# Optimization experiments

Hardware: AMD Instinct MI355X
Metric: run time of the kernel (lower is better)

Reference implementation:

```python
import jax, jax.numpy as jnp
import numpy as np

N_NODES = 100000


def _mean_agg(feat, src, dst, n):
    # segment mean of neighbor messages: h_N[v] = mean_{(u->v) in E} feat[u]
    s = jax.ops.segment_sum(feat[src], dst, num_segments=n)  # [n, d]
    cnt = jax.ops.segment_sum(jnp.ones_like(src, dtype=feat.dtype), dst, num_segments=n)
    return s / jnp.maximum(cnt, 1.0)[:, None]  # isolated nodes -> 0 (DGL mean gives 0)


def setup_inputs() -> dict:
    key = jax.random.key(0)
    k1, k2, k3, k4, k5 = jax.random.split(key, 5)
    n, d_in, d_hid, d_out, n_edges = N_NODES, 128, 128, 64, 1600000
    feat = jax.random.normal(k1, (n, d_in), dtype=jnp.float32)
    edge_src = jax.random.randint(k2, (n_edges,), 0, n, dtype=jnp.int32)
    edge_dst = jax.random.randint(k3, (n_edges,), 0, n, dtype=jnp.int32)
    # xavier_uniform with relu gain, torch Linear weight layout [out, in]
    gain = float(np.sqrt(2.0))
    def xavier(k, out_f, in_f):
        bound = gain * np.sqrt(6.0 / (in_f + out_f))
        return jax.random.uniform(k, (out_f, in_f), minval=-bound, maxval=bound, dtype=jnp.float32)
    W0 = xavier(k4, d_hid, 2 * d_in)
    W1 = xavier(k5, d_out, 2 * d_hid)
    return {"feat": feat, "edge_src": edge_src, "edge_dst": edge_dst, "W0": W0, "W1": W1}


def reference(feat, edge_src, edge_dst, W0, W1):
    n = feat.shape[0]
    # layer 0: mean-aggregate, concat, linear, relu (dropout p=0 -> identity)
    h_N = _mean_agg(feat, edge_src, edge_dst, n)
    h = jax.nn.relu(jnp.concatenate([feat, h_N], axis=1) @ W0.T)
    # final layer: mean-aggregate, concat, linear (no relu)
    h_N2 = _mean_agg(h, edge_src, edge_dst, n)
    out = jnp.concatenate([h, h_N2], axis=1) @ W1.T
    return out
```

## Files before the change

kernel.cpp:

```cpp
#include <hip/hip_runtime.h>
#include <hip/hip_bf16.h>

typedef __attribute__((ext_vector_type(8))) short bf16x8;
typedef __attribute__((ext_vector_type(4))) float f32x4;
typedef __attribute__((ext_vector_type(2))) float f32x2;

#define BSH 9
#define BCAP 12288

#if __has_builtin(__builtin_amdgcn_cvt_pk_f32_fp8) && __has_builtin(__builtin_amdgcn_cvt_pk_fp8_f32)
#define FP8_HW 1
#else
#define FP8_HW 0
#endif

__device__ __forceinline__ float bf2f(unsigned short u) {
    return __uint_as_float(((unsigned int)u) << 16);
}
__device__ __forceinline__ unsigned short f2bf(float f) {
    unsigned int u = __float_as_uint(f);
    unsigned int r = u + 0x7FFFu + ((u >> 16) & 1u);
    return (unsigned short)(r >> 16);
}
__device__ __forceinline__ unsigned int pack2bf(float a, float b) {
    return (unsigned int)f2bf(a) | ((unsigned int)f2bf(b) << 16);
}

#if !FP8_HW
__device__ __forceinline__ unsigned int f2fp8_sw(float v) {
    unsigned int u = __float_as_uint(v);
    unsigned int s = (u >> 24) & 0x80u;
    unsigned int a = u & 0x7FFFFFFFu;
    float av = __uint_as_float(a);
    unsigned int q;
    if (av >= 0.015625f) {
        unsigned int r = a + 0x7FFFFu + ((a >> 20) & 1u);
        q = (r - (120u << 23)) >> 20;
        if (q > 0x7Eu) q = 0x7Eu;
    } else {
        q = (unsigned int)(av * 512.0f + 0.5f);
    }
    return s | q;
}
__device__ __forceinline__ float fp8_dec_sw(unsigned int u8) {
    unsigned int s = (u8 & 0x80u) << 24;
    unsigned int em = u8 & 0x7Fu;
    float vn = __uint_as_float(s | ((em << 20) + (120u << 23)));
    float vs = __uint_as_float(s | 0x3B000000u) * (float)(int)em;
    return em >= 8 ? vn : vs;
}
#endif

__device__ __forceinline__ void fp8x4_dec(unsigned int d, float& x, float& y, float& z, float& w) {
#if FP8_HW
    f32x2 lo = __builtin_amdgcn_cvt_pk_f32_fp8((int)d, false);
    f32x2 hi = __builtin_amdgcn_cvt_pk_f32_fp8((int)d, true);
    x = lo.x; y = lo.y; z = hi.x; w = hi.y;
#else
    x = fp8_dec_sw(d & 0xFFu);
    y = fp8_dec_sw((d >> 8) & 0xFFu);
    z = fp8_dec_sw((d >> 16) & 0xFFu);
    w = fp8_dec_sw((d >> 24) & 0xFFu);
#endif
}
__device__ __forceinline__ unsigned int fp8x4_enc(float a, float b, float c, float d) {
#if FP8_HW
    int u = __builtin_amdgcn_cvt_pk_fp8_f32(a, b, 0, false);
    u = __builtin_amdgcn_cvt_pk_fp8_f32(c, d, u, true);
    return (unsigned int)u;
#else
    return f2fp8_sw(a) | (f2fp8_sw(b) << 8) | (f2fp8_sw(c) << 16) | (f2fp8_sw(d) << 24);
#endif
}
__device__ __forceinline__ unsigned char fp8_enc1(float a) {
#if FP8_HW
    return (unsigned char)(__builtin_amdgcn_cvt_pk_fp8_f32(a, a, 0, false) & 0xFF);
#else
    return (unsigned char)f2fp8_sw(a);
#endif
}

__global__ __launch_bounds__(256) void megaA(const int* __restrict__ esrc, const int* __restrict__ edst,
                                             int* __restrict__ gcur, unsigned int* __restrict__ pairs,
                                             int E, int NB,
                                             const float* __restrict__ feat,
                                             unsigned char* __restrict__ Ff8, int nquad,
                                             const float* __restrict__ W0, unsigned short* __restrict__ Wb1,
                                             const float* __restrict__ W1, unsigned short* __restrict__ Wb2,
                                             int pblocks, int cblocks) {
    __shared__ int bcnt[256];
    __shared__ int bbas[256];
    int b = blockIdx.x, t = threadIdx.x;
    if (b < pblocks) {
        int e0 = b * 4096;
        int eend = min(e0 + 4096, E);
        if (t < NB) bcnt[t] = 0;
        __syncthreads();
        for (int e = e0 + t; e < eend; e += 256) atomicAdd(&bcnt[edst[e] >> BSH], 1);
        __syncthreads();
        if (t < NB) {
            bbas[t] = t * BCAP + atomicAdd(&gcur[t], bcnt[t]);
            bcnt[t] = 0;
        }
        __syncthreads();
        for (int e = e0 + t; e < eend; e += 256) {
            int d = edst[e];
            int s = esrc[e];
            int bk = d >> BSH;
            int off = atomicAdd(&bcnt[bk], 1);
            pairs[bbas[bk] + off] = (unsigned int)s | ((unsigned int)(d & ((1 << BSH) - 1)) << 17);
        }
    } else if (b < pblocks + cblocks) {
        int cb = b - pblocks;
        for (int q = cb * 256 + t; q < nquad; q += cblocks * 256) {
            float4 f = *(const float4*)(feat + (size_t)q * 4);
            *(unsigned int*)(Ff8 + (size_t)q * 4) = fp8x4_enc(f.x, f.y, f.z, f.w);
        }
    } else {
        int wb = b - pblocks - cblocks;
        for (int i = wb * 256 + t; i < 49152; i += 24 * 256) {
            if (i < 32768) {
                Wb1[i] = f2bf(W0[i]);
            } else {
                int i2 = i - 32768;
                int j = i2 >> 7, k = i2 & 127;
                float vv = (j < 64) ? W1[j * 256 + k] : W1[(j - 64) * 256 + 128 + k];
                Wb2[i2] = f2bf(vv);
            }
        }
    }
}

__global__ __launch_bounds__(256) void build(const unsigned int* __restrict__ pairs,
                                             const int* __restrict__ gcur,
                                             int* __restrict__ offs, int* __restrict__ csr,
                                             int n, int NB, int E) {
    __shared__ int cnt[512];
    __shared__ int excl[512];
    __shared__ int wsum[4];
    __shared__ int woff[4];
    __shared__ int sbase;
    int b = blockIdx.x, t = threadIdx.x, lane = t & 63, wv = t >> 6;

    {
        int vv = (t < NB) ? gcur[t] : 0;
        int x = vv;
#pragma unroll
        for (int o = 1; o < 64; o <<= 1) {
            int y = __shfl_up(x, o, 64);
            if (lane >= o) x += y;
        }
        if (lane == 63) wsum[wv] = x;
        __syncthreads();
        if (t == 0) {
            int r = 0;
            for (int w = 0; w < 4; ++w) { woff[w] = r; r += wsum[w]; }
        }
        __syncthreads();
        if (t == b) sbase = woff[wv] + x - vv;
        if (b == 0 && t == 0) offs[n] = E;
    }
    __syncthreads();
    int base = sbase;
    int p0 = b * BCAP;
    int m = gcur[b];
    int v0 = b << BSH;

    cnt[t] = 0;
    cnt[t + 256] = 0;
    __syncthreads();
    for (int i = t; i < m; i += 256) atomicAdd(&cnt[pairs[p0 + i] >> 17], 1);
    __syncthreads();
    int c0 = cnt[2 * t], c1 = cnt[2 * t + 1];
    int s = c0 + c1;
    int x = s;
#pragma unroll
    for (int o = 1; o < 64; o <<= 1) {
        int y = __shfl_up(x, o, 64);
        if (lane >= o) x += y;
    }
    if (lane == 63) wsum[wv] = x;
    __syncthreads();
    if (t == 0) {
        int r = 0;
        for (int w = 0; w < 4; ++w) { woff[w] = r; r += wsum[w]; }
    }
    __syncthreads();
    int ex = woff[wv] + x - s;
    excl[2 * t] = ex;
    excl[2 * t + 1] = ex + c0;
    int v = v0 + 2 * t;
    if (v + 1 < n) {
        int2 o2;
        o2.x = base + ex;
        o2.y = base + ex + c0;
        *(int2*)(offs + v) = o2;
    } else if (v < n) {
        offs[v] = base + ex;
    }
    cnt[t] = 0;
    cnt[t + 256] = 0;
    __syncthreads();
    for (int i = t; i < m; i += 256) {
        unsigned int u = pairs[p0 + i];
        int dl = u >> 17;
        int off = atomicAdd(&cnt[dl], 1);
        csr[base + excl[dl] + off] = (int)(u & 0x1FFFFu);
    }
}

__global__ __launch_bounds__(256) void agg1(const unsigned char* __restrict__ Ff8,
                                            const int* __restrict__ offs,
                                            const int* __restrict__ csr,
                                            unsigned short* __restrict__ Mb, int n) {
    int t = threadIdx.x;
    int hw = t >> 5, cl = t & 31;
    int v = blockIdx.x * 8 + hw;
    if (v >= n) return;
    int beg = offs[v], end = offs[v + 1];
    float a0 = 0.f, a1 = 0.f, a2 = 0.f, a3 = 0.f;
    int e = beg;
    for (; e + 7 < end; e += 8) {
        int s[8];
#pragma unroll
        for (int k = 0; k < 8; ++k) s[k] = csr[e + k];
        unsigned int d[8];
#pragma unroll
        for (int k = 0; k < 8; ++k)
            d[k] = *(const unsigned int*)(Ff8 + (size_t)s[k] * 128 + cl * 4);
#pragma unroll
        for (int k = 0; k < 8; ++k) {
            float x, y, z, w2;
            fp8x4_dec(d[k], x, y, z, w2);
            a0 += x; a1 += y; a2 += z; a3 += w2;
        }
    }
    for (; e < end; ++e) {
        unsigned int d0 = *(const unsigned int*)(Ff8 + (size_t)csr[e] * 128 + cl * 4);
        float x, y, z, w2;
        fp8x4_dec(d0, x, y, z, w2);
        a0 += x; a1 += y; a2 += z; a3 += w2;
    }
    int deg = end - beg;
    float inv = 1.0f / (float)(deg > 0 ? deg : 1);
    uint2 pk;
    pk.x = pack2bf(a0 * inv, a1 * inv);
    pk.y = pack2bf(a2 * inv, a3 * inv);
    *(uint2*)(Mb + (size_t)v * 128 + cl * 4) = pk;
}

__global__ __launch_bounds__(256) void fused_gemm(const float* __restrict__ feat,
                                                  const unsigned short* __restrict__ Mb,
                                                  const unsigned short* __restrict__ Wb1,
                                                  const unsigned short* __restrict__ Wc,
                                                  unsigned short* __restrict__ Za,
                                                  unsigned char* __restrict__ Zb8,
                                                  int n) {
    __shared__ __align__(16) unsigned char smem[32768];
    int t = threadIdx.x, l = t & 63, w = t >> 6;
    int m0 = blockIdx.x * 128;
    int lr = l & 15;
    int lk = (l >> 4) * 8;
    int rbase = (l >> 4) * 4;

    f32x4 acc2[2][8];
    {
        f32x4 acc[2][8];
#pragma unroll
        for (int m = 0; m < 2; ++m)
#pragma unroll
            for (int nf = 0; nf < 8; ++nf) acc[m][nf] = (f32x4){0.f, 0.f, 0.f, 0.f};
#pragma unroll
        for (int kc = 0; kc < 8; ++kc) {
            int kb = kc * 32 + lk;
            bf16x8 a[2];
#pragma unroll
            for (int m = 0; m < 2; ++m) {
                int grow = m0 + w * 32 + m * 16 + lr;
                grow = (grow < n) ? grow : (n - 1);
                if (kb < 128) {
                    float4 f0 = *(const float4*)(feat + (size_t)grow * 128 + kb);
                    float4 f1 = *(const float4*)(feat + (size_t)grow * 128 + kb + 4);
                    uint4 pk;
                    pk.x = pack2bf(f0.x, f0.y);
                    pk.y = pack2bf(f0.z, f0.w);
                    pk.z = pack2bf(f1.x, f1.y);
                    pk.w = pack2bf(f1.z, f1.w);
                    a[m] = *(const bf16x8*)&pk;
                } else {
                    a[m] = *(const bf16x8*)(Mb + (size_t)grow * 128 + (kb - 128));
                }
            }
            bf16x8 bfr[8];
#pragma unroll
            for (int nf = 0; nf < 8; ++nf)
                bfr[nf] = *(const bf16x8*)(Wb1 + (size_t)(nf * 16 + lr) * 256 + kb);
#pragma unroll
            for (int m = 0; m < 2; ++m)
#pragma unroll
                for (int nf = 0; nf < 8; ++nf)
                    acc[m][nf] = __builtin_amdgcn_mfma_f32_16x16x32_bf16(a[m], bfr[nf], acc[m][nf], 0, 0, 0);
        }
#pragma unroll
        for (int m = 0; m < 2; ++m)
#pragma unroll
            for (int nf = 0; nf < 8; ++nf)
#pragma unroll
                for (int r = 0; r < 4; ++r) {
                    int row = w * 32 + m * 16 + rbase + r;
                    int cb = (nf * 16 + lr) * 2;
                    *(unsigned short*)(smem + row * 256 + (cb ^ ((row & 7) << 4))) =
                        f2bf(fmaxf(acc[m][nf][r], 0.f));
                }

#pragma unroll
        for (int m = 0; m < 2; ++m)
#pragma unroll
            for (int nf = 0; nf < 8; ++nf) acc2[m][nf] = (f32x4){0.f, 0.f, 0.f, 0.f};
#pragma unroll
        for (int kc = 0; kc < 4; ++kc) {
            int kb = kc * 32 + lk;
            int cb = kb * 2;
            bf16x8 a[2];
#pragma unroll
            for (int m = 0; m < 2; ++m) {
                int row = w * 32 + m * 16 + lr;
                a[m] = *(const bf16x8*)(smem + row * 256 + (cb ^ ((row & 7) << 4)));
            }
            bf16x8 bfr[8];
#pragma unroll
            for (int nf = 0; nf < 8; ++nf)
                bfr[nf] = *(const bf16x8*)(Wc + (size_t)(nf * 16 + lr) * 128 + kb);
#pragma unroll
            for (int m = 0; m < 2; ++m)
#pragma unroll
                for (int nf = 0; nf < 8; ++nf)
                    acc2[m][nf] = __builtin_amdgcn_mfma_f32_16x16x32_bf16(a[m], bfr[nf], acc2[m][nf], 0, 0, 0);
        }
    }
    __syncthreads();

    {
        unsigned char* zaT = smem;
        unsigned char* zbT = smem + 16384;
#pragma unroll
        for (int m = 0; m < 2; ++m)
#pragma unroll
            for (int nf = 0; nf < 8; ++nf)
#pragma unroll
                for (int r = 0; r < 4; ++r) {
                    float vv = acc2[m][nf][r];
                    int row = w * 32 + m * 16 + rbase + r;
                    if (nf < 4)
                        *(unsigned short*)(zaT + row * 128 + (nf * 16 + lr) * 2) = f2bf(vv);
                    else
                        zbT[row * 64 + (nf - 4) * 16 + lr] = fp8_enc1(vv);
                }
    }
    __syncthreads();

#pragma unroll
    for (int c = 0; c < 4; ++c) {
        int chunk = c * 256 + t;
        int row = chunk >> 3, cb = (chunk & 7) * 16;
        int grow = m0 + row;
        if (grow < n)
            *(uint4*)((unsigned char*)Za + (size_t)grow * 128 + cb) = *(const uint4*)(smem + row * 128 + cb);
    }
#pragma unroll
    for (int c = 0; c < 2; ++c) {
        int chunk = c * 256 + t;
        int row = chunk >> 2, cb = (chunk & 3) * 16;
        int grow = m0 + row;
        if (grow < n)
            *(uint4*)(Zb8 + (size_t)grow * 64 + cb) = *(const uint4*)(smem + 16384 + row * 64 + cb);
    }
}

__global__ __launch_bounds__(256) void agg2(const unsigned short* __restrict__ Za,
                                            const unsigned char* __restrict__ Zb8,
                                            const int* __restrict__ offs,
                                            const int* __restrict__ csr,
                                            float* __restrict__ out, int n) {
    int t = threadIdx.x;
    int q = t >> 4, cl = t & 15;
    int v = blockIdx.x * 16 + q;
    if (v >= n) return;
    int beg = offs[v], end = offs[v + 1];
    float a0 = 0.f, a1 = 0.f, a2 = 0.f, a3 = 0.f;
    int e = beg;
    for (; e + 7 < end; e += 8) {
        int s[8];
#pragma unroll
        for (int k = 0; k < 8; ++k) s[k] = csr[e + k];
        unsigned int d[8];
#pragma unroll
        for (int k = 0; k < 8; ++k)
            d[k] = *(const unsigned int*)(Zb8 + (size_t)s[k] * 64 + cl * 4);
#pragma unroll
        for (int k = 0; k < 8; ++k) {
            float x, y, z, u2;
            fp8x4_dec(d[k], x, y, z, u2);
            a0 += x; a1 += y; a2 += z; a3 += u2;
        }
    }
    for (; e < end; ++e) {
        unsigned int d0 = *(const unsigned int*)(Zb8 + (size_t)csr[e] * 64 + cl * 4);
        float x, y, z, u2;
        fp8x4_dec(d0, x, y, z, u2);
        a0 += x; a1 += y; a2 += z; a3 += u2;
    }
    int deg = end - beg;
    float inv = 1.0f / (float)(deg > 0 ? deg : 1);
    uint2 uz = *(const uint2*)((const unsigned char*)Za + (size_t)v * 128 + cl * 8);
    float4 o;
    o.x = bf2f((unsigned short)uz.x) + a0 * inv;
    o.y = bf2f((unsigned short)(uz.x >> 16)) + a1 * inv;
    o.z = bf2f((unsigned short)uz.y) + a2 * inv;
    o.w = bf2f((unsigned short)(uz.y >> 16)) + a3 * inv;
    *(float4*)(out + (size_t)v * 64 + cl * 4) = o;
}

extern "C" void kernel_launch(void* const* d_in, const int* in_sizes, int n_in,
                              void* d_out, int out_size, void* d_ws, size_t ws_size,
                              hipStream_t stream) {
    const float* feat = (const float*)d_in[0];
    const int* esrc = (const int*)d_in[1];
    const int* edst = (const int*)d_in[2];
    const float* W0 = (const float*)d_in[3];
    const float* W1 = (const float*)d_in[4];
    float* out = (float*)d_out;

    int n = in_sizes[0] / 128;
    int E = in_sizes[1];
    int NB = (n + 511) >> 9;

    char* ws = (char*)d_ws;
    size_t off = 0;
    auto alloc = [&](size_t bytes) -> void* {
        void* p = ws + off;
        off += (bytes + 255) & ~(size_t)255;
        return p;
    };
    int* offs = (int*)alloc((size_t)(n + 1) * 4);
    int* csr = (int*)alloc((size_t)E * 4);
    int* gcur = (int*)alloc((size_t)NB * 4);
    unsigned int* pairs = (unsigned int*)alloc((size_t)NB * BCAP * 4);
    unsigned short* Wb1 = (unsigned short*)alloc((size_t)128 * 256 * 2);
    unsigned short* Wb2 = (unsigned short*)alloc((size_t)128 * 128 * 2);
    unsigned char* Ff8 = (unsigned char*)alloc((size_t)n * 128);
    unsigned short* Mb = (unsigned short*)alloc((size_t)n * 128 * 2);
    unsigned short* Za = (unsigned short*)alloc((size_t)n * 64 * 2);
    unsigned char* Zb8 = (unsigned char*)alloc((size_t)n * 64);

    int pblocks = (E + 4095) / 4096;
    int cblocks = 640;
    int nquad = n * 32;

    hipMemsetAsync(gcur, 0, (size_t)NB * 4, stream);
    megaA<<<pblocks + cblocks + 24, 256, 0, stream>>>(esrc, edst, gcur, pairs, E, NB,
                                                      feat, Ff8, nquad,
                                                      W0, Wb1, W1, Wb2, pblocks, cblocks);
    build<<<NB, 256, 0, stream>>>(pairs, gcur, offs, csr, n, NB, E);

    agg1<<<(n + 7) / 8, 256, 0, stream>>>(Ff8, offs, csr, Mb, n);
    fused_gemm<<<(n + 127) / 128, 256, 0, stream>>>(feat, Mb, Wb1, Wb2, Za, Zb8, n);
    agg2<<<(n + 15) / 16, 256, 0, stream>>>(Za, Zb8, offs, csr, out, n);
}
```

Baseline: 190.9 us.

## Precompute bf16 features and restructure fused GEMM with transposed MFMA and 64-row tiles

The feature-conversion pass now also writes a bf16 copy of the input features, so the fused GEMM reads bf16 directly instead of converting fp32 per tile. The GEMM is restructured to use 64-node tiles with one 16-row fragment per wave, swapping MFMA operands so weights are the A operand. This lets results be packed as contiguous vectors into swizzled shared memory, and the output staging now uses packed fp8 encoding. It adds an extra bf16 feature buffer, which costs one more write and read of the features, while halving shared memory and doubling the block count.

```diff
diff --git a/kernel.cpp b/kernel.cpp
--- a/kernel.cpp
+++ b/kernel.cpp
@@ -72,18 +72,11 @@
     return f2fp8_sw(a) | (f2fp8_sw(b) << 8) | (f2fp8_sw(c) << 16) | (f2fp8_sw(d) << 24);
 #endif
 }
-__device__ __forceinline__ unsigned char fp8_enc1(float a) {
-#if FP8_HW
-    return (unsigned char)(__builtin_amdgcn_cvt_pk_fp8_f32(a, a, 0, false) & 0xFF);
-#else
-    return (unsigned char)f2fp8_sw(a);
-#endif
-}
 
 __global__ __launch_bounds__(256) void megaA(const int* __restrict__ esrc, const int* __restrict__ edst,
                                              int* __restrict__ gcur, unsigned int* __restrict__ pairs,
                                              int E, int NB,
-                                             const float* __restrict__ feat,
+                                             const float* __restrict__ feat, unsigned short* __restrict__ Fb,
                                              unsigned char* __restrict__ Ff8, int nquad,
                                              const float* __restrict__ W0, unsigned short* __restrict__ Wb1,
                                              const float* __restrict__ W1, unsigned short* __restrict__ Wb2,
@@ -114,6 +107,9 @@
         int cb = b - pblocks;
         for (int q = cb * 256 + t; q < nquad; q += cblocks * 256) {
             float4 f = *(const float4*)(feat + (size_t)q * 4);
+            ushort4 ub;
+            ub.x = f2bf(f.x); ub.y = f2bf(f.y); ub.z = f2bf(f.z); ub.w = f2bf(f.w);
+            *(ushort4*)(Fb + (size_t)q * 4) = ub;
             *(unsigned int*)(Ff8 + (size_t)q * 4) = fp8x4_enc(f.x, f.y, f.z, f.w);
         }
     } else {
@@ -249,131 +245,109 @@
     *(uint2*)(Mb + (size_t)v * 128 + cl * 4) = pk;
 }
 
-__global__ __launch_bounds__(256) void fused_gemm(const float* __restrict__ feat,
+__global__ __launch_bounds__(256) void fused_gemm(const unsigned short* __restrict__ Fb,
                                                   const unsigned short* __restrict__ Mb,
                                                   const unsigned short* __restrict__ Wb1,
                                                   const unsigned short* __restrict__ Wc,
                                                   unsigned short* __restrict__ Za,
                                                   unsigned char* __restrict__ Zb8,
                                                   int n) {
-    __shared__ __align__(16) unsigned char smem[32768];
+    __shared__ __align__(16) unsigned char smem[16384];
     int t = threadIdx.x, l = t & 63, w = t >> 6;
-    int m0 = blockIdx.x * 128;
+    int m0 = blockIdx.x * 64;
     int lr = l & 15;
-    int lk = (l >> 4) * 8;
+    int lk8 = (l >> 4) * 8;
     int rbase = (l >> 4) * 4;
 
-    f32x4 acc2[2][8];
-    {
-        f32x4 acc[2][8];
-#pragma unroll
-        for (int m = 0; m < 2; ++m)
-#pragma unroll
-            for (int nf = 0; nf < 8; ++nf) acc[m][nf] = (f32x4){0.f, 0.f, 0.f, 0.f};
-#pragma unroll
-        for (int kc = 0; kc < 8; ++kc) {
-            int kb = kc * 32 + lk;
-            bf16x8 a[2];
-#pragma unroll
-            for (int m = 0; m < 2; ++m) {
-                int grow = m0 + w * 32 + m * 16 + lr;
-                grow = (grow < n) ? grow : (n - 1);
-                if (kb < 128) {
-                    float4 f0 = *(const float4*)(feat + (size_t)grow * 128 + kb);
-                    float4 f1 = *(const float4*)(feat + (size_t)grow * 128 + kb + 4);
-                    uint4 pk;
-                    pk.x = pack2bf(f0.x, f0.y);
-                    pk.y = pack2bf(f0.z, f0.w);
-                    pk.z = pack2bf(f1.x, f1.y);
-                    pk.w = pack2bf(f1.z, f1.w);
-                    a[m] = *(const bf16x8*)&pk;
-                } else {
-                    a[m] = *(const bf16x8*)(Mb + (size_t)grow * 128 + (kb - 128));
-                }
-            }
-            bf16x8 bfr[8];
-#pragma unroll
-            for (int nf = 0; nf < 8; ++nf)
-                bfr[nf] = *(const bf16x8*)(Wb1 + (size_t)(nf * 16 + lr) * 256 + kb);
-#pragma unroll
-            for (int m = 0; m < 2; ++m)
-#pragma unroll
-                for (int nf = 0; nf < 8; ++nf)
-                    acc[m][nf] = __builtin_amdgcn_mfma_f32_16x16x32_bf16(a[m], bfr[nf], acc[m][nf], 0, 0, 0);
-        }
-#pragma unroll
-        for (int m = 0; m < 2; ++m)
-#pragma unroll
-            for (int nf = 0; nf < 8; ++nf)
-#pragma unroll
-                for (int r = 0; r < 4; ++r) {
-                    int row = w * 32 + m * 16 + rbase + r;
-                    int cb = (nf * 16 + lr) * 2;
-                    *(unsigned short*)(smem + row * 256 + (cb ^ ((row & 7) << 4))) =
-                        f2bf(fmaxf(acc[m][nf][r], 0.f));
-                }
-
-#pragma unroll
-        for (int m = 0; m < 2; ++m)
-#pragma unroll
-            for (int nf = 0; nf < 8; ++nf) acc2[m][nf] = (f32x4){0.f, 0.f, 0.f, 0.f};
-#pragma unroll
-        for (int kc = 0; kc < 4; ++kc) {
-            int kb = kc * 32 + lk;
-            int cb = kb * 2;
-            bf16x8 a[2];
-#pragma unroll
-            for (int m = 0; m < 2; ++m) {
-                int row = w * 32 + m * 16 + lr;
-                a[m] = *(const bf16x8*)(smem + row * 256 + (cb ^ ((row & 7) << 4)));
-            }
-            bf16x8 bfr[8];
-#pragma unroll
-            for (int nf = 0; nf < 8; ++nf)
-                bfr[nf] = *(const bf16x8*)(Wc + (size_t)(nf * 16 + lr) * 128 + kb);
-#pragma unroll
-            for (int m = 0; m < 2; ++m)
-#pragma unroll
-                for (int nf = 0; nf < 8; ++nf)
-                    acc2[m][nf] = __builtin_amdgcn_mfma_f32_16x16x32_bf16(a[m], bfr[nf], acc2[m][nf], 0, 0, 0);
-        }
+    int ln = w * 16 + lr;
+    int node = m0 + ln;
+    int nclamp = (node < n) ? node : (n - 1);
+    unsigned int sw = (unsigned int)((ln & 7) << 4);
+    unsigned char* hrow = smem + ln * 256;
+
+    f32x4 acc[8];
+#pragma unroll
+    for (int of = 0; of < 8; ++of) acc[of] = (f32x4){0.f, 0.f, 0.f, 0.f};
+#pragma unroll
+    for (int kc = 0; kc < 8; ++kc) {
+        int kb = kc * 32 + lk8;
+        bf16x8 x;
+        if (kb < 128)
+            x = *(const bf16x8*)(Fb + (size_t)nclamp * 128 + kb);
+        else
+            x = *(const bf16x8*)(Mb + (size_t)nclamp * 128 + (kb - 128));
+        bf16x8 wf[8];
+#pragma unroll
+        for (int of = 0; of < 8; ++of)
+            wf[of] = *(const bf16x8*)(Wb1 + (size_t)(of * 16 + lr) * 256 + kb);
+#pragma unroll
+        for (int of = 0; of < 8; ++of)
+            acc[of] = __builtin_amdgcn_mfma_f32_16x16x32_bf16(wf[of], x, acc[of], 0, 0, 0);
+    }
+#pragma unroll
+    for (int of = 0; of < 8; ++of) {
+        uint2 pk;
+        pk.x = pack2bf(fmaxf(acc[of][0], 0.f), fmaxf(acc[of][1], 0.f));
+        pk.y = pack2bf(fmaxf(acc[of][2], 0.f), fmaxf(acc[of][3], 0.f));
+        unsigned int ob = (unsigned int)(of * 32 + rbase * 2);
+        *(uint2*)(hrow + (ob ^ sw)) = pk;
+    }
+
+    f32x4 acc2[8];
+#pragma unroll
+    for (int of = 0; of < 8; ++of) acc2[of] = (f32x4){0.f, 0.f, 0.f, 0.f};
+#pragma unroll
+    for (int kc = 0; kc < 4; ++kc) {
+        int kb = kc * 32 + lk8;
+        unsigned int kbyte = (unsigned int)(kb * 2);
+        bf16x8 x = *(const bf16x8*)(hrow + (kbyte ^ sw));
+        bf16x8 wf[8];
+#pragma unroll
+        for (int of = 0; of < 8; ++of)
+            wf[of] = *(const bf16x8*)(Wc + (size_t)(of * 16 + lr) * 128 + kb);
+#pragma unroll
+        for (int of = 0; of < 8; ++of)
+            acc2[of] = __builtin_amdgcn_mfma_f32_16x16x32_bf16(wf[of], x, acc2[of], 0, 0, 0);
     }
     __syncthreads();
 
     {
         unsigned char* zaT = smem;
-        unsigned char* zbT = smem + 16384;
-#pragma unroll
-        for (int m = 0; m < 2; ++m)
-#pragma unroll
-            for (int nf = 0; nf < 8; ++nf)
-#pragma unroll
-                for (int r = 0; r < 4; ++r) {
-                    float vv = acc2[m][nf][r];
-                    int row = w * 32 + m * 16 + rbase + r;
-                    if (nf < 4)
-                        *(unsigned short*)(zaT + row * 128 + (nf * 16 + lr) * 2) = f2bf(vv);
-                    else
-                        zbT[row * 64 + (nf - 4) * 16 + lr] = fp8_enc1(vv);
-                }
-    }
-    __syncthreads();
-
-#pragma unroll
-    for (int c = 0; c < 4; ++c) {
+        unsigned char* zbT = smem + 8192;
+        unsigned int swa = (unsigned int)((ln & 7) << 4);
+        unsigned int swb = (unsigned int)((ln & 3) << 4);
+#pragma unroll
+        for (int of = 0; of < 4; ++of) {
+            uint2 pk;
+            pk.x = pack2bf(acc2[of][0], acc2[of][1]);
+            pk.y = pack2bf(acc2[of][2], acc2[of][3]);
+            unsigned int ob = (unsigned int)(of * 32 + rbase * 2);
+            *(uint2*)(zaT + ln * 128 + (ob ^ swa)) = pk;
+        }
+#pragma unroll
+        for (int of = 4; of < 8; ++of) {
+            unsigned int pk = fp8x4_enc(acc2[of][0], acc2[of][1], acc2[of][2], acc2[of][3]);
+            unsigned int ob = (unsigned int)((of - 4) * 16 + rbase);
+            *(unsigned int*)(zbT + ln * 64 + (ob ^ swb)) = pk;
+        }
+    }
+    __syncthreads();
+
+#pragma unroll
+    for (int c = 0; c < 2; ++c) {
         int chunk = c * 256 + t;
         int row = chunk >> 3, cb = (chunk & 7) * 16;
         int grow = m0 + row;
         if (grow < n)
-            *(uint4*)((unsigned char*)Za + (size_t)grow * 128 + cb) = *(const uint4*)(smem + row * 128 + cb);
-    }
-#pragma unroll
-    for (int c = 0; c < 2; ++c) {
-        int chunk = c * 256 + t;
-        int row = chunk >> 2, cb = (chunk & 3) * 16;
+            *(uint4*)((unsigned char*)Za + (size_t)grow * 128 + cb) =
+                *(const uint4*)(smem + row * 128 + (cb ^ ((row & 7) << 4)));
+    }
+    {
+        int row = t >> 2, cb = (t & 3) * 16;
         int grow = m0 + row;
         if (grow < n)
-            *(uint4*)(Zb8 + (size_t)grow * 64 + cb) = *(const uint4*)(smem + 16384 + row * 64 + cb);
+            *(uint4*)(Zb8 + (size_t)grow * 64 + cb) =
+                *(const uint4*)(smem + 8192 + row * 64 + (cb ^ ((row & 3) << 4)));
     }
 }
 
@@ -448,6 +422,7 @@
     unsigned int* pairs = (unsigned int*)alloc((size_t)NB * BCAP * 4);
     unsigned short* Wb1 = (unsigned short*)alloc((size_t)128 * 256 * 2);
     unsigned short* Wb2 = (unsigned short*)alloc((size_t)128 * 128 * 2);
+    unsigned short* Fb = (unsigned short*)alloc((size_t)n * 128 * 2);
     unsigned char* Ff8 = (unsigned char*)alloc((size_t)n * 128);
     unsigned short* Mb = (unsigned short*)alloc((size_t)n * 128 * 2);
     unsigned short* Za = (unsigned short*)alloc((size_t)n * 64 * 2);
@@ -459,11 +434,11 @@
 
     hipMemsetAsync(gcur, 0, (size_t)NB * 4, stream);
     megaA<<<pblocks + cblocks + 24, 256, 0, stream>>>(esrc, edst, gcur, pairs, E, NB,
-                                                      feat, Ff8, nquad,
+                                                      feat, Fb, Ff8, nquad,
                                                       W0, Wb1, W1, Wb2, pblocks, cblocks);
     build<<<NB, 256, 0, stream>>>(pairs, gcur, offs, csr, n, NB, E);
 
     agg1<<<(n + 7) / 8, 256, 0, stream>>>(Ff8, offs, csr, Mb, n);
-    fused_gemm<<<(n + 127) / 128, 256, 0, stream>>>(feat, Mb, Wb1, Wb2, Za, Zb8, n);
+    fused_gemm<<<(n + 63) / 64, 256, 0, stream>>>(Fb, Mb, Wb1, Wb2, Za, Zb8, n);
     agg2<<<(n + 15) / 16, 256, 0, stream>>>(Za, Zb8, offs, csr, out, n);
 }
```

New measurement: 218.9 us. 14.6% more time.
